# Optimization experiments

Hardware: AMD Instinct MI355X
Metric: run time of the kernel (lower is better)

Reference implementation:

```python
import jax, jax.numpy as jnp
import numpy as np

N_AGENTS = 8
N_ACTIONS = 14
STATE_DIM = 168
RNN_DIM = 64
GAT_DIM = 32
N_HEADS = 4
HYPER = 64


def setup_inputs() -> dict:
    key = jax.random.key(0)
    ks = jax.random.split(key, 16)
    bs, T = 256, 256
    def xavier(k, shape):
        fan_in, fan_out = shape[0], shape[-1]
        lim = float(np.sqrt(6.0 / (fan_in + fan_out)))
        return jax.random.uniform(k, shape, jnp.float32, -lim, lim)
    return {
        'agent_qs': jax.random.normal(ks[0], (bs, T, N_AGENTS), jnp.float32),
        'states': jax.random.normal(ks[1], (bs, T, STATE_DIM), jnp.float32),
        'max_q_i': jax.random.normal(ks[2], (bs, T, N_AGENTS), jnp.float32),
        'hidden_states': jax.random.normal(ks[3], (bs, T, N_AGENTS, RNN_DIM), jnp.float32),
        # hyper_w_final MLP
        'w1f': xavier(ks[4], (STATE_DIM, HYPER)), 'b1f': jnp.zeros((HYPER,), jnp.float32),
        'w2f': xavier(ks[5], (HYPER, N_AGENTS)), 'b2f': jnp.zeros((N_AGENTS,), jnp.float32),
        # V MLP
        'w1v': xavier(ks[6], (STATE_DIM, HYPER)), 'b1v': jnp.zeros((HYPER,), jnp.float32),
        'w2v': xavier(ks[7], (HYPER, N_AGENTS)), 'b2v': jnp.zeros((N_AGENTS,), jnp.float32),
        # GAT: W (no bias) and attention vector att_a [1, H, 2*d]
        'Wg': xavier(ks[8], (RNN_DIM, N_HEADS * GAT_DIM)),
        'att_a': xavier(ks[9], (1, N_HEADS, 2 * GAT_DIM)) * 1.414,
        # hyper_w_dvd linear
        'Wd': xavier(ks[10], (STATE_DIM, N_HEADS * GAT_DIM)), 'bd': jnp.zeros((N_HEADS * GAT_DIM,), jnp.float32),
    }


def reference(agent_qs, states, max_q_i, hidden_states,
              w1f, b1f, w2f, b2f, w1v, b1v, w2v, b2v,
              Wg, att_a, Wd, bd):
    bs = agent_qs.shape[0]
    S = states.reshape(-1, STATE_DIM)                     # [B, state_dim]
    q = agent_qs.reshape(-1, N_AGENTS)                    # [B, n]
    mq = max_q_i.reshape(-1, N_AGENTS)
    H = hidden_states.reshape(-1, N_AGENTS, RNN_DIM)      # [B, n, rnn]

    # weighted_head=True branch
    w_final = jnp.abs(jax.nn.relu(S @ w1f + b1f) @ w2f + b2f) + 1e-10
    v = jax.nn.relu(S @ w1v + b1v) @ w2v + b2v
    q = w_final * q + v
    mq = w_final * mq + v
    adv_q = jax.lax.stop_gradient(q - mq)                 # .detach() in torch

    # MultiHeadGAT on tiny agent graph, without materializing h_cat
    hp = jnp.einsum('bni,ihd->bhnd', H, Wg.reshape(RNN_DIM, N_HEADS, GAT_DIM))  # [B,h,n,d]
    a_i = att_a[0, :, :GAT_DIM]                           # [h, d]
    a_j = att_a[0, :, GAT_DIM:]
    e_i = jnp.einsum('bhnd,hd->bhn', hp, a_i)
    e_j = jnp.einsum('bhnd,hd->bhn', hp, a_j)
    e = e_i[:, :, :, None] + e_j[:, :, None, :]           # [B,h,n,n]
    e = jnp.where(e > 0, e, 0.2 * e)                      # LeakyReLU(0.2)
    attn = jax.nn.softmax(e, axis=-1)
    graphs = jax.nn.elu(jnp.einsum('bhij,bhjd->bhid', attn, hp))  # [B,h,n,d]

    # DVD weights
    w_dvd = (S @ Wd + bd).reshape(-1, N_HEADS, GAT_DIM)   # [B,h,d]
    weights_dvd = jnp.abs(jnp.einsum('bhd,bhnd->bhn', w_dvd, graphs))  # [B,h,n]
    adv_w_final = weights_dvd.mean(axis=1)                # [B,n]

    # is_minus_one=True
    adv_tot = jnp.sum(adv_q * (adv_w_final - 1.0), axis=1)
    return adv_tot.reshape(bs, -1, 1)
```

## Files before the change

### kernel.cpp

```cpp
#include <hip/hip_runtime.h>
#include <math.h>

#define STATE_DIM 168
#define BTOT 65536
#define SLS 1064
#define SPAD 184

typedef float f32x4 __attribute__((ext_vector_type(4)));
typedef short bf16x8 __attribute__((ext_vector_type(8)));

union Frag { bf16x8 v; unsigned short u[8]; };
union Acc  { f32x4 v; float f[4]; };

__device__ __forceinline__ unsigned short f2bf(float f) {
    unsigned int u = __float_as_uint(f);
    u += 0x7fffu + ((u >> 16) & 1u);
    return (unsigned short)(u >> 16);
}

__global__ void __launch_bounds__(256, 3)
fused_kernel(const float* __restrict__ states,
             const float* __restrict__ w1f, const float* __restrict__ b1f,
             const float* __restrict__ w2f, const float* __restrict__ b2f,
             const float* __restrict__ Wd,  const float* __restrict__ bd,
             const float* __restrict__ agent_qs,
             const float* __restrict__ max_q_i,
             const float* __restrict__ hidden,
             const float* __restrict__ Wg,
             const float* __restrict__ att_a,
             float* __restrict__ out)
{
    __shared__ float hp_lds[4][2 * SLS];
    __shared__ float e_lds[4][128];
    __shared__ float ws_lds[4][64];
    __shared__ float a_lds[264];
    __shared__ float wdvd_lds[32 * 144];
    __shared__ float wfin_lds[32 * 8];

    unsigned short* S_bf = (unsigned short*)&hp_lds[0][0];
    float*          y1   = &hp_lds[2][0];

    const int t    = threadIdx.x;
    const int wid  = t >> 6;
    const int lane = t & 63;
    const int quad = lane >> 4;
    const int col  = lane & 15;

    {
        const int h = t >> 6, r = t & 63, wch = r >> 5, d = r & 31;
        a_lds[(h * 2 + wch) * 33 + d] = att_a[t];
    }

    const long blk0 = (long)blockIdx.x * 32;

    {
        Frag B[3][6];
        #pragma unroll
        for (int ks = 0; ks < 6; ++ks)
            #pragma unroll
            for (int j = 0; j < 8; ++j) {
                const int k = ks * 32 + quad * 8 + j;
                const bool v = (k < STATE_DIM);
                B[0][ks].u[j] = v ? f2bf(w1f[k * 64 + wid * 16 + col]) : (unsigned short)0;
                B[1][ks].u[j] = v ? f2bf(Wd[k * 128 + wid * 32 + col]) : (unsigned short)0;
                B[2][ks].u[j] = v ? f2bf(Wd[k * 128 + wid * 32 + 16 + col]) : (unsigned short)0;
            }
        Frag B2[2];
        #pragma unroll
        for (int ks = 0; ks < 2; ++ks)
            #pragma unroll
            for (int j = 0; j < 8; ++j) {
                const int k = ks * 32 + quad * 8 + j;
                B2[ks].u[j] = (col < 8) ? f2bf(w2f[k * 8 + col]) : (unsigned short)0;
            }

        const float bias1  = b1f[wid * 16 + col];
        const float biasd0 = bd[wid * 32 + col];
        const float biasd1 = bd[wid * 32 + 16 + col];
        const float bias2  = (col < 8) ? b2f[col] : 0.0f;

        for (int it = 0; it < 2; ++it) {
            const long smp0 = blk0 + it * 16;

            {
                const int r = t >> 4, u = t & 15;
                const float* Srow = states + (smp0 + r) * STATE_DIM;
                #pragma unroll
                for (int i = 0; i < 12; ++i) {
                    const int k = u + 16 * i;
                    if (k < SPAD) {
                        unsigned short vv = (k < STATE_DIM) ? f2bf(Srow[k])
                                                            : (unsigned short)0;
                        S_bf[r * SPAD + k] = vv;
                    }
                }
            }
            __syncthreads();

            Frag A[6];
            #pragma unroll
            for (int ks = 0; ks < 6; ++ks) {
                int k0 = ks * 32 + quad * 8;
                if (ks == 5 && quad != 0) k0 = STATE_DIM;
                A[ks].v = *(const bf16x8*)&S_bf[col * SPAD + k0];
            }

            Acc D0, D1, D2t;
            D0.v = (f32x4){0.f,0.f,0.f,0.f};
            D1.v = (f32x4){0.f,0.f,0.f,0.f};
            D2t.v = (f32x4){0.f,0.f,0.f,0.f};
            #pragma unroll
            for (int ks = 0; ks < 6; ++ks) {
                D0.v  = __builtin_amdgcn_mfma_f32_16x16x32_bf16(A[ks].v, B[0][ks].v, D0.v, 0, 0, 0);
                D1.v  = __builtin_amdgcn_mfma_f32_16x16x32_bf16(A[ks].v, B[1][ks].v, D1.v, 0, 0, 0);
                D2t.v = __builtin_amdgcn_mfma_f32_16x16x32_bf16(A[ks].v, B[2][ks].v, D2t.v, 0, 0, 0);
            }

            #pragma unroll
            for (int r = 0; r < 4; ++r) {
                const int m = quad * 4 + r;
                const int l = it * 16 + m;
                y1[m * 72 + wid * 16 + col] = fmaxf(D0.f[r] + bias1, 0.0f);
                wdvd_lds[l * 144 + wid * 36 + col]      = D1.f[r]  + biasd0;
                wdvd_lds[l * 144 + wid * 36 + 16 + col] = D2t.f[r] + biasd1;
            }
            __syncthreads();

            {
                Frag A2[2];
                #pragma unroll
                for (int ks = 0; ks < 2; ++ks) {
                    const float4 p0 = *(const float4*)&y1[col * 72 + ks * 32 + quad * 8];
                    const float4 p1 = *(const float4*)&y1[col * 72 + ks * 32 + quad * 8 + 4];
                    A2[ks].u[0] = f2bf(p0.x); A2[ks].u[1] = f2bf(p0.y);
                    A2[ks].u[2] = f2bf(p0.z); A2[ks].u[3] = f2bf(p0.w);
                    A2[ks].u[4] = f2bf(p1.x); A2[ks].u[5] = f2bf(p1.y);
                    A2[ks].u[6] = f2bf(p1.z); A2[ks].u[7] = f2bf(p1.w);
                }
                Acc Dw;
                Dw.v = (f32x4){0.f,0.f,0.f,0.f};
                Dw.v = __builtin_amdgcn_mfma_f32_16x16x32_bf16(A2[0].v, B2[0].v, Dw.v, 0, 0, 0);
                Dw.v = __builtin_amdgcn_mfma_f32_16x16x32_bf16(A2[1].v, B2[1].v, Dw.v, 0, 0, 0);
                if (wid == 0 && col < 8) {
                    #pragma unroll
                    for (int r = 0; r < 4; ++r)
                        wfin_lds[(it * 16 + quad * 4 + r) * 8 + col] =
                            fabsf(Dw.f[r] + bias2) + 1e-10f;
                }
            }
            __syncthreads();
        }
    }

    {
        float* hp  = hp_lds[wid];
        float* el  = e_lds[wid];
        float* wsl = ws_lds[wid];

        Frag Bf[8][2];
        #pragma unroll
        for (int tt = 0; tt < 8; ++tt)
            #pragma unroll
            for (int ks = 0; ks < 2; ++ks)
                #pragma unroll
                for (int j = 0; j < 8; ++j)
                    Bf[tt][ks].u[j] =
                        f2bf(Wg[(ks * 32 + quad * 8 + j) * 128 + tt * 16 + col]);

        const int sl_a = (lane >> 3) & 1;
        const int n_a  = lane & 7;
        const int sl_w = quad >> 1;
        const int nb   = (quad & 1) * 4;

        for (int g = 0; g < 4; ++g) {
            const int  l0   = wid * 8 + 2 * g;
            const long smp0 = blk0 + l0;

            Frag A0, A1;
            {
                const float* Hb = hidden + (smp0 + sl_a) * 512 + n_a * 64 + quad * 8;
                const float4 h00 = *(const float4*)(Hb);
                const float4 h01 = *(const float4*)(Hb + 4);
                const float4 h10 = *(const float4*)(Hb + 32);
                const float4 h11 = *(const float4*)(Hb + 36);
                A0.u[0] = f2bf(h00.x); A0.u[1] = f2bf(h00.y);
                A0.u[2] = f2bf(h00.z); A0.u[3] = f2bf(h00.w);
                A0.u[4] = f2bf(h01.x); A0.u[5] = f2bf(h01.y);
                A0.u[6] = f2bf(h01.z); A0.u[7] = f2bf(h01.w);
                A1.u[0] = f2bf(h10.x); A1.u[1] = f2bf(h10.y);
                A1.u[2] = f2bf(h10.z); A1.u[3] = f2bf(h10.w);
                A1.u[4] = f2bf(h11.x); A1.u[5] = f2bf(h11.y);
                A1.u[6] = f2bf(h11.z); A1.u[7] = f2bf(h11.w);
            }

            #pragma unroll
            for (int tt = 0; tt < 8; ++tt) {
                Acc acc;
                acc.v = (f32x4){0.f, 0.f, 0.f, 0.f};
                acc.v = __builtin_amdgcn_mfma_f32_16x16x32_bf16(A0.v, Bf[tt][0].v, acc.v, 0, 0, 0);
                acc.v = __builtin_amdgcn_mfma_f32_16x16x32_bf16(A1.v, Bf[tt][1].v, acc.v, 0, 0, 0);
                const int c = tt * 16 + col;
                float4 st = {acc.f[0], acc.f[1], acc.f[2], acc.f[3]};
                *(float4*)&hp[sl_w * SLS + c * 8 + ((c >> 5) << 3) + nb] = st;
            }

            {
                const int h = lane >> 4, r = lane & 15, wch = r >> 3, n = r & 7;
                const float* arow = &a_lds[(h * 2 + wch) * 33];
                #pragma unroll
                for (int sl = 0; sl < 2; ++sl) {
                    float acc = 0.f;
                    #pragma unroll
                    for (int d = 0; d < 32; ++d)
                        acc = fmaf(hp[sl * SLS + (h * 32 + d) * 8 + h * 8 + n],
                                   arow[d], acc);
                    el[sl * 64 + wch * 32 + h * 8 + n] = acc;
                }
            }

            {
                const int sl = lane >> 5, r = lane & 31, h = r >> 3, n = r & 7;
                const long smp = smp0 + sl;

                float at8[8];
                {
                    const float eiv = el[sl * 64 + h * 8 + n];
                    const float* ejp = &el[sl * 64 + 32 + h * 8];
                    float mx = -1e30f;
                    #pragma unroll
                    for (int j = 0; j < 8; ++j) {
                        float v = eiv + ejp[j];
                        v = v > 0.f ? v : 0.2f * v;
                        at8[j] = v;
                        mx = fmaxf(mx, v);
                    }
                    float ssum = 0.f;
                    #pragma unroll
                    for (int j = 0; j < 8; ++j) { at8[j] = __expf(at8[j] - mx); ssum += at8[j]; }
                    const float inv = 1.f / ssum;
                    #pragma unroll
                    for (int j = 0; j < 8; ++j) at8[j] *= inv;
                }

                float wdd[32];
                {
                    const float* wdp = &wdvd_lds[(l0 + sl) * 144 + h * 36];
                    #pragma unroll
                    for (int q4 = 0; q4 < 8; ++q4) {
                        const float4 v = *(const float4*)(wdp + q4 * 4);
                        wdd[q4 * 4 + 0] = v.x; wdd[q4 * 4 + 1] = v.y;
                        wdd[q4 * 4 + 2] = v.z; wdd[q4 * 4 + 3] = v.w;
                    }
                }
                float part = 0.f;
                #pragma unroll
                for (int d = 0; d < 32; ++d) {
                    const int c = h * 32 + d;
                    const float* hb = &hp[sl * SLS + c * 8 + h * 8];
                    const float4 p0 = *(const float4*)(hb);
                    const float4 p1 = *(const float4*)(hb + 4);
                    float gg = at8[0] * p0.x;
                    gg = fmaf(at8[1], p0.y, gg);
                    gg = fmaf(at8[2], p0.z, gg);
                    gg = fmaf(at8[3], p0.w, gg);
                    gg = fmaf(at8[4], p1.x, gg);
                    gg = fmaf(at8[5], p1.y, gg);
                    gg = fmaf(at8[6], p1.z, gg);
                    gg = fmaf(at8[7], p1.w, gg);
                    gg = gg > 0.f ? gg : (__expf(gg) - 1.0f);
                    part = fmaf(wdd[d], gg, part);
                }
                wsl[sl * 32 + h * 8 + n] = fabsf(part);
            }

            {
                const int sl = lane >> 5, r = lane & 31;
                if (r < 8) {
                    const int n = r;
                    const long smp = smp0 + sl;
                    const int  l   = l0 + sl;
                    const float awf = 0.25f * (wsl[sl * 32 + n] + wsl[sl * 32 + 8 + n] +
                                               wsl[sl * 32 + 16 + n] + wsl[sl * 32 + 24 + n]);
                    const float adv = wfin_lds[l * 8 + n] *
                                      (agent_qs[smp * 8 + n] - max_q_i[smp * 8 + n]);
                    float p = adv * (awf - 1.0f);
                    p += __shfl_xor(p, 4, 64);
                    p += __shfl_xor(p, 2, 64);
                    p += __shfl_xor(p, 1, 64);
                    if (n == 0) out[smp] = p;
                }
            }
        }
    }
}

extern "C" void kernel_launch(void* const* d_in, const int* in_sizes, int n_in,
                              void* d_out, int out_size, void* d_ws, size_t ws_size,
                              hipStream_t stream) {
    const float* agent_qs = (const float*)d_in[0];
    const float* states   = (const float*)d_in[1];
    const float* max_q_i  = (const float*)d_in[2];
    const float* hidden   = (const float*)d_in[3];
    const float* w1f = (const float*)d_in[4];
    const float* b1f = (const float*)d_in[5];
    const float* w2f = (const float*)d_in[6];
    const float* b2f = (const float*)d_in[7];
    const float* Wg    = (const float*)d_in[12];
    const float* att_a = (const float*)d_in[13];
    const float* Wd    = (const float*)d_in[14];
    const float* bd    = (const float*)d_in[15];
    float* out  = (float*)d_out;

    (void)d_ws; (void)ws_size;

    fused_kernel<<<2048, 256, 0, stream>>>(states, w1f, b1f, w2f, b2f, Wd, bd,
                                           agent_qs, max_q_i, hidden, Wg, att_a,
                                           out);
}
```

Before: 318.5 us.

## Cut LDS footprint: keep att_a in registers, shuffle-reduce heads, tighten padding

Loads the attention vector into per-lane registers instead of staging it in shared memory, and replaces the ws_lds round trip for the cross-head mean with two lane shuffles. It also shrinks the wdvd row stride and the hp slab padding and reads w_dvd directly from LDS inside the dot loop instead of preloading 32 values into registers. Together these reduce shared memory and register use, which may allow more resident blocks. The trade-off is extra register pressure from areg, and the new strides (odd 33-float head stride) may change LDS bank-conflict behaviour.

```diff
diff --git a/kernel.cpp b/kernel.cpp
--- a/kernel.cpp
+++ b/kernel.cpp
@@ -3,7 +3,7 @@
 
 #define STATE_DIM 168
 #define BTOT 65536
-#define SLS 1064
+#define SLS 1048
 #define SPAD 184
 
 typedef float f32x4 __attribute__((ext_vector_type(4)));
@@ -32,9 +32,7 @@
 {
     __shared__ float hp_lds[4][2 * SLS];
     __shared__ float e_lds[4][128];
-    __shared__ float ws_lds[4][64];
-    __shared__ float a_lds[264];
-    __shared__ float wdvd_lds[32 * 144];
+    __shared__ float wdvd_lds[32 * 132];
     __shared__ float wfin_lds[32 * 8];
 
     unsigned short* S_bf = (unsigned short*)&hp_lds[0][0];
@@ -45,11 +43,6 @@
     const int lane = t & 63;
     const int quad = lane >> 4;
     const int col  = lane & 15;
-
-    {
-        const int h = t >> 6, r = t & 63, wch = r >> 5, d = r & 31;
-        a_lds[(h * 2 + wch) * 33 + d] = att_a[t];
-    }
 
     const long blk0 = (long)blockIdx.x * 32;
 
@@ -121,8 +114,8 @@
                 const int m = quad * 4 + r;
                 const int l = it * 16 + m;
                 y1[m * 72 + wid * 16 + col] = fmaxf(D0.f[r] + bias1, 0.0f);
-                wdvd_lds[l * 144 + wid * 36 + col]      = D1.f[r]  + biasd0;
-                wdvd_lds[l * 144 + wid * 36 + 16 + col] = D2t.f[r] + biasd1;
+                wdvd_lds[l * 132 + wid * 33 + col]      = D1.f[r]  + biasd0;
+                wdvd_lds[l * 132 + wid * 33 + 16 + col] = D2t.f[r] + biasd1;
             }
             __syncthreads();
 
@@ -155,7 +148,18 @@
     {
         float* hp  = hp_lds[wid];
         float* el  = e_lds[wid];
-        float* wsl = ws_lds[wid];
+
+        float areg[32];
+        {
+            const int h_a = lane >> 4, wch_a = (lane & 15) >> 3;
+            const float* ap = att_a + h_a * 64 + wch_a * 32;
+            #pragma unroll
+            for (int q = 0; q < 8; ++q) {
+                const float4 v = *(const float4*)(ap + q * 4);
+                areg[q * 4 + 0] = v.x; areg[q * 4 + 1] = v.y;
+                areg[q * 4 + 2] = v.z; areg[q * 4 + 3] = v.w;
+            }
+        }
 
         Frag Bf[8][2];
         #pragma unroll
@@ -206,14 +210,13 @@
 
             {
                 const int h = lane >> 4, r = lane & 15, wch = r >> 3, n = r & 7;
-                const float* arow = &a_lds[(h * 2 + wch) * 33];
                 #pragma unroll
                 for (int sl = 0; sl < 2; ++sl) {
                     float acc = 0.f;
                     #pragma unroll
                     for (int d = 0; d < 32; ++d)
                         acc = fmaf(hp[sl * SLS + (h * 32 + d) * 8 + h * 8 + n],
-                                   arow[d], acc);
+                                   areg[d], acc);
                     el[sl * 64 + wch * 32 + h * 8 + n] = acc;
                 }
             }
@@ -242,16 +245,7 @@
                     for (int j = 0; j < 8; ++j) at8[j] *= inv;
                 }
 
-                float wdd[32];
-                {
-                    const float* wdp = &wdvd_lds[(l0 + sl) * 144 + h * 36];
-                    #pragma unroll
-                    for (int q4 = 0; q4 < 8; ++q4) {
-                        const float4 v = *(const float4*)(wdp + q4 * 4);
-                        wdd[q4 * 4 + 0] = v.x; wdd[q4 * 4 + 1] = v.y;
-                        wdd[q4 * 4 + 2] = v.z; wdd[q4 * 4 + 3] = v.w;
-                    }
-                }
+                const float* wdp = &wdvd_lds[(l0 + sl) * 132 + h * 33];
                 float part = 0.f;
                 #pragma unroll
                 for (int d = 0; d < 32; ++d) {
@@ -268,19 +262,16 @@
                     gg = fmaf(at8[6], p1.z, gg);
                     gg = fmaf(at8[7], p1.w, gg);
                     gg = gg > 0.f ? gg : (__expf(gg) - 1.0f);
-                    part = fmaf(wdd[d], gg, part);
-                }
-                wsl[sl * 32 + h * 8 + n] = fabsf(part);
-            }
-
-            {
-                const int sl = lane >> 5, r = lane & 31;
+                    part = fmaf(wdp[d], gg, part);
+                }
+
+                float pa = fabsf(part);
+                pa += __shfl_xor(pa, 8, 64);
+                pa += __shfl_xor(pa, 16, 64);
+
                 if (r < 8) {
-                    const int n = r;
-                    const long smp = smp0 + sl;
-                    const int  l   = l0 + sl;
-                    const float awf = 0.25f * (wsl[sl * 32 + n] + wsl[sl * 32 + 8 + n] +
-                                               wsl[sl * 32 + 16 + n] + wsl[sl * 32 + 24 + n]);
+                    const int l = l0 + sl;
+                    const float awf = 0.25f * pa;
                     const float adv = wfin_lds[l * 8 + n] *
                                       (agent_qs[smp * 8 + n] - max_q_i[smp * 8 + n]);
                     float p = adv * (awf - 1.0f);
```

New measurement: 331.1 us. 3.9% more time.
